# Kernel optimization log

Hardware: AMD Instinct MI355X
Metric: run time of the kernel (lower is better)

Reference implementation:

```python
import jax, jax.numpy as jnp
import numpy as np

DIM = 64
LSH_NUM_PROJS = 7
BLOCK_SIZE = 256
SAMPLE_SIZE = 256
MIN_SEQ_LEN = 2048


def _unit_hamming(n):
    # Gray-code-like permutation used by AngularLSH so adjacent hash ids differ by 1 bit
    a = np.arange(2)
    for i in range(1, n):
        a = np.concatenate([a, a[::-1] + 2 ** i])
    return jnp.asarray(a, dtype=jnp.int32)

_PERM = _unit_hamming(LSH_NUM_PROJS)                                  # [2^P]
_ENC = (2 ** jnp.arange(LSH_NUM_PROJS)).reshape(1, 1, 1, LSH_NUM_PROJS)


def _lsh_hash(mat, proj_dir):
    # mat: [b,h,n,d], proj_dir: [1,1,d,P] -> hash ids [b,h,n]
    mask = jnp.matmul(mat, proj_dir) > 0
    bin_ids = (mask * _ENC).sum(-1)
    return _PERM[bin_ids]


def _exact_attention(q, k, v, scale, causal=False, bias=None):
    qk = jnp.einsum('bhnd,bhmd->bhnm', q, k) * scale
    if causal:
        n, m = q.shape[2], k.shape[2]
        qk = qk + jnp.triu(jnp.full((n, m), jnp.finfo(q.dtype).min, q.dtype), 1)[None, None]
    if bias is not None:
        qk = qk + bias
    lse = jax.scipy.special.logsumexp(qk, axis=-1, keepdims=True)      # [b,h,n,1]
    out = jnp.einsum('bhnm,bhmd->bhnd', jnp.exp(qk - lse), v)
    return out, lse


def _add_attn(a1, l1, a2, l2):
    c = (1.0 / (1.0 + jnp.exp(l2 - l1))).astype(a1.dtype)
    attn = c * a1 + (1 - c) * a2
    lse = l1 - jnp.log(c + jnp.finfo(l1.dtype).eps)
    return attn, lse


def _indexing(x, idx, chunk_size=-1):
    # x: [b,h,n,d], idx: [b,h,s] -> [b,h,s,d] (padded up to a multiple of chunk_size)
    g = jnp.take_along_axis(x, idx[..., None], axis=2)
    n = g.shape[2]
    if chunk_size > 0 and n % chunk_size != 0:
        pad = -n % chunk_size
        g = jnp.pad(g, ((0, 0), (0, 0), (0, pad), (0, 0)))
    return g


def _no_causal(q, k, v, scale, proj_dir, level):
    b, h, n_q, d = q.shape
    n_k = k.shape[2]
    if MIN_SEQ_LEN > n_q:
        return _exact_attention(q, k, v, scale, causal=False)
    q_idx = jnp.argsort(_lsh_hash(q, proj_dir), axis=2)
    k_idx = jnp.argsort(_lsh_hash(k, proj_dir), axis=2)
    q_idx_inv = jnp.argsort(q_idx, axis=2)
    kbs = BLOCK_SIZE
    q_s = _indexing(q, q_idx, kbs)
    k_s = _indexing(k, k_idx, kbs)
    v_s = _indexing(v, k_idx, kbs)
    num_blocks = k_s.shape[2] // kbs
    qbs = q_s.shape[2] // num_blocks
    # block-diagonal attention over LSH-sorted buckets
    q_blk = q_s.reshape(-1, 1, qbs, d)
    k_blk = k_s.reshape(-1, 1, kbs, d)
    v_blk = v_s.reshape(-1, 1, kbs, d)
    attn_block, lse_block = _exact_attention(q_blk, k_blk, v_blk, scale, causal=False)
    attn_block = attn_block.reshape(b, h, q_s.shape[2], -1)
    lse_block = lse_block.reshape(b, h, q_s.shape[2], -1)
    if q_s.shape[2] != n_q:
        attn_block = attn_block[:, :, :n_q, :]
        lse_block = lse_block[:, :, :n_q, :]
        q_s = q_s[:, :, :n_q, :]
        k_s = k_s[:, :, :n_k, :]
        v_s = v_s[:, :, :n_k, :]
    S = SAMPLE_SIZE
    if S > 0 and n_q > qbs and n_k > kbs:
        rng = jax.random.fold_in(jax.random.key(42), level)
        sampled = jax.random.randint(rng, (b, h, S), 0, n_k)
        v_sub = _indexing(v_s, sampled)
        k_sub = _indexing(k_s, sampled)
        offset = jnp.arange(n_q)[None, :, None]                         # (1,n,1)
        bm = (offset // qbs) == (sampled // kbs).reshape(-1, 1, S)      # (b*h,n,S)
        bias = bm.reshape(b, h, n_q, S).astype(q_s.dtype) * jnp.finfo(q_s.dtype).min
        attn_res, lse_res = _exact_attention(q_s, k_sub, v_sub, scale, causal=False, bias=bias)
        lse_res = lse_res + jnp.asarray(np.log(n_k / S), lse_res.dtype)
        attn, lse = _add_attn(attn_block, lse_block, attn_res, lse_res)
    else:
        attn, lse = attn_block, lse_block
    attn = _indexing(attn, q_idx_inv)
    lse = _indexing(lse, q_idx_inv)
    return attn, lse


def _hyper(q, k, v, scale, proj_dir, level=0):
    b, h, n_k, d = k.shape
    n_q = q.shape[2]
    if n_k <= MIN_SEQ_LEN:
        return _exact_attention(q, k, v, scale, causal=True)
    # recursive causal split: block-diagonal halves + un-masked lower-left quadrant
    q_bd = q.reshape(b, 2 * h, n_q // 2, d)
    k_bd = k.reshape(b, 2 * h, n_k // 2, d)
    v_bd = v.reshape(b, 2 * h, n_k // 2, d)
    attn_bd, lse_bd = _hyper(q_bd, k_bd, v_bd, scale, proj_dir, level + 1)
    attn_bd = attn_bd.reshape(b, h, -1, d)
    lse_bd = lse_bd.reshape(b, h, -1, 1)
    a_un, l_un = _no_causal(q[:, :, n_k // 2:, :], k[:, :, :n_k // 2, :],
                            v[:, :, :n_k // 2, :], scale, proj_dir, 100 + level)
    a_up, l_up = attn_bd[:, :, :n_q // 2, :], lse_bd[:, :, :n_q // 2, :]
    a_dn, l_dn = _add_attn(attn_bd[:, :, n_q // 2:, :], lse_bd[:, :, n_q // 2:, :], a_un, l_un)
    return jnp.concatenate([a_up, a_dn], axis=2), jnp.concatenate([l_up, l_dn], axis=2)


def setup_inputs() -> dict:
    rng = jax.random.key(0)
    kq, kk, kv, kp = jax.random.split(rng, 4)
    B, H, N, D = 1, 8, 8192, 64
    return {
        'query': jax.random.normal(kq, (B, H, N, D), jnp.float32),
        'key': jax.random.normal(kk, (B, H, N, D), jnp.float32),
        'value': jax.random.normal(kv, (B, H, N, D), jnp.float32),
        'proj_dir': jax.random.normal(kp, (1, 1, D, LSH_NUM_PROJS), jnp.float32),
    }


def reference(query, key, value, proj_dir):
    scale = query.shape[-1] ** -0.5
    attn, lse = _hyper(query, key, value, scale, proj_dir)
    return attn
```

## Files before the change

kernel.cpp:

```cpp
#include <hip/hip_runtime.h>
#include <stdint.h>
#include <math.h>

#define H 8
#define NSEQ 8192
#define D 64
#define SC2 0.18033688011112042f
#define LN2F 0.69314718055994531f
#define THR2 10.0f
#define EPSF 1.1920928955078125e-07f

typedef short v8s __attribute__((ext_vector_type(8)));
typedef float v4f __attribute__((ext_vector_type(4)));
typedef unsigned short ushort_t;

#define MFMA16(a,b,c) __builtin_amdgcn_mfma_f32_16x16x32_bf16((a),(b),(c),0,0,0)
#define SWZ(row, cb)    (((row)*128) + ((cb) ^ ((((row)&7))<<4)))
#define SWZ256(row, cb) (((row)*256) + ((cb) ^ ((((row)&7))<<4)))

__device__ __forceinline__ float exp2x(float x){
  float r; asm("v_exp_f32 %0, %1" : "=v"(r) : "v"(x)); return r;
}
__device__ __forceinline__ unsigned int cvtpk(float a, float b){
  unsigned int r; asm("v_cvt_pk_bf16_f32 %0, %1, %2" : "=v"(r) : "v"(a), "v"(b)); return r;
}
__device__ __forceinline__ ushort_t f2bf(float f){
  union { float f; unsigned int u; } c; c.f = f;
  unsigned int u = c.u + 0x7FFFu + ((c.u >> 16) & 1u);
  return (ushort_t)(u >> 16);
}
#define VONES (v8s){0x3F80,0x3F80,0x3F80,0x3F80,0x3F80,0x3F80,0x3F80,0x3F80}

__global__ __launch_bounds__(256) void prep_hash(
    const float* __restrict__ q, const float* __restrict__ k, const float* __restrict__ v,
    const float* __restrict__ proj,
    ushort_t* __restrict__ qb, ushort_t* __restrict__ kb, ushort_t* __restrict__ vb,
    int* __restrict__ hq, int* __restrict__ hk)
{
  __shared__ float tile[64][65];
  __shared__ float pj[448];
  __shared__ int pbuf[4][64];
  const int bid = blockIdx.x;
  const int t = threadIdx.x;
  if (bid >= 2048){
    const int tix = bid - 2048;
    size_t off = (size_t)tix*4096 + t*16;
    float4 f0 = *(const float4*)(v + off);
    float4 f1 = *(const float4*)(v + off + 4);
    float4 f2 = *(const float4*)(v + off + 8);
    float4 f3 = *(const float4*)(v + off + 12);
    uint4 o0, o1;
    o0.x = cvtpk(f0.x, f0.y);  o0.y = cvtpk(f0.z, f0.w);
    o0.z = cvtpk(f1.x, f1.y);  o0.w = cvtpk(f1.z, f1.w);
    o1.x = cvtpk(f2.x, f2.y);  o1.y = cvtpk(f2.z, f2.w);
    o1.z = cvtpk(f3.x, f3.y);  o1.w = cvtpk(f3.z, f3.w);
    *(uint4*)(vb + off) = o0;
    *(uint4*)(vb + off + 8) = o1;
    return;
  }
  const int isk = bid & 1;
  const int tix = bid >> 1;
  const int rowbase = tix << 6;
  const float* src = isk ? k : q;
  ushort_t* dstb = isk ? kb : qb;
  int* dsth = isk ? hk : hq;
  for (int i = t; i < 448; i += 256) pj[i] = proj[i];
  {
    const int r = t >> 2, cg = (t & 3) << 4;
    const float* s = src + (size_t)(rowbase + r)*64 + cg;
    float4 f0 = *(const float4*)(s);
    float4 f1 = *(const float4*)(s + 4);
    float4 f2 = *(const float4*)(s + 8);
    float4 f3 = *(const float4*)(s + 12);
    tile[r][cg+0]=f0.x;  tile[r][cg+1]=f0.y;  tile[r][cg+2]=f0.z;  tile[r][cg+3]=f0.w;
    tile[r][cg+4]=f1.x;  tile[r][cg+5]=f1.y;  tile[r][cg+6]=f1.z;  tile[r][cg+7]=f1.w;
    tile[r][cg+8]=f2.x;  tile[r][cg+9]=f2.y;  tile[r][cg+10]=f2.z; tile[r][cg+11]=f2.w;
    tile[r][cg+12]=f3.x; tile[r][cg+13]=f3.y; tile[r][cg+14]=f3.z; tile[r][cg+15]=f3.w;
    uint4 o0, o1;
    o0.x = cvtpk(f0.x, f0.y);  o0.y = cvtpk(f0.z, f0.w);
    o0.z = cvtpk(f1.x, f1.y);  o0.w = cvtpk(f1.z, f1.w);
    o1.x = cvtpk(f2.x, f2.y);  o1.y = cvtpk(f2.z, f2.w);
    o1.z = cvtpk(f3.x, f3.y);  o1.w = cvtpk(f3.z, f3.w);
    *(uint4*)(dstb + (size_t)(rowbase + r)*64 + cg) = o0;
    *(uint4*)(dstb + (size_t)(rowbase + r)*64 + cg + 8) = o1;
  }
  __syncthreads();
  {
    const int r = t & 63, pg = t >> 6;
    const int p2 = (pg < 3) ? (pg + 4) : 6;
    float d0 = 0.0f, d1 = 0.0f;
    for (int d = 0; d < 64; ++d){
      float x = tile[r][d];
      d0 = fmaf(x, pj[d*7 + pg], d0);
      d1 = fmaf(x, pj[d*7 + p2], d1);
    }
    int pb = (d0 > 0.0f ? (1 << pg) : 0);
    if (pg < 3 && d1 > 0.0f) pb |= (1 << (pg + 4));
    pbuf[pg][r] = pb;
  }
  __syncthreads();
  if (t < 64){
    int b = pbuf[0][t] | pbuf[1][t] | pbuf[2][t] | pbuf[3][t];
    dsth[rowbase + t] = b ^ (b >> 1);
  }
}

__device__ __forceinline__ void tf2x32(uint32_t k0, uint32_t k1,
                                       uint32_t x0, uint32_t x1,
                                       uint32_t& o0, uint32_t& o1)
{
  uint32_t ks0 = k0, ks1 = k1, ks2 = k0 ^ k1 ^ 0x1BD11BDAu;
  x0 += ks0; x1 += ks1;
#define RND(r) { x0 += x1; x1 = (x1 << (r)) | (x1 >> (32-(r))); x1 ^= x0; }
  RND(13) RND(15) RND(26) RND(6)  x0 += ks1; x1 += ks2 + 1u;
  RND(17) RND(29) RND(16) RND(24) x0 += ks2; x1 += ks0 + 2u;
  RND(13) RND(15) RND(26) RND(6)  x0 += ks0; x1 += ks1 + 3u;
  RND(17) RND(29) RND(16) RND(24) x0 += ks1; x1 += ks2 + 4u;
  RND(13) RND(15) RND(26) RND(6)  x0 += ks2; x1 += ks0 + 5u;
#undef RND
  o0 = x0; o1 = x1;
}

__device__ __forceinline__ void qk8(const v8s qf[2], const char* Ks, int lo, int hi, v4f sa[8]){
  __builtin_amdgcn_s_setprio(1);
#pragma unroll
  for (int st = 0; st < 8; ++st){
#pragma unroll
    for (int kc = 0; kc < 2; ++kc){
      v8s bf = *(const v8s*)(Ks + SWZ(st*16 + lo, kc*64 + hi*16));
      sa[st] = MFMA16(qf[kc], bf, sa[st]);
    }
  }
  __builtin_amdgcn_s_setprio(0);
}

__device__ __forceinline__ void sm_pv8s(v4f sa[8], char* Pw, const char* VTs,
                                        int lo, int hi, float m[4], v4f o[5]){
  float tm[4];
  bool grow = false;
#pragma unroll
  for (int reg = 0; reg < 4; ++reg){
    float a = fmaxf(fmaxf(sa[0][reg], sa[1][reg]), fmaxf(sa[2][reg], sa[3][reg]));
    float b = fmaxf(fmaxf(sa[4][reg], sa[5][reg]), fmaxf(sa[6][reg], sa[7][reg]));
    tm[reg] = fmaxf(a, b);
    grow = grow || (tm[reg] > m[reg] + THR2);
  }
  if (__any(grow)){
#pragma unroll
    for (int reg = 0; reg < 4; ++reg){
      float t = tm[reg];
      t = fmaxf(t, __shfl_xor(t, 1));
      t = fmaxf(t, __shfl_xor(t, 2));
      t = fmaxf(t, __shfl_xor(t, 4));
      t = fmaxf(t, __shfl_xor(t, 8));
      float mn = fmaxf(m[reg], t);
      float corr = exp2x(m[reg] - mn);
      m[reg] = mn;
#pragma unroll
      for (int dt = 0; dt < 5; ++dt) o[dt][reg] *= corr;
    }
  }
#pragma unroll
  for (int hh = 0; hh < 2; ++hh){
#pragma unroll
    for (int reg = 0; reg < 4; ++reg){
      float mr = m[reg];
      uint2 pw;
      pw.x = cvtpk(exp2x(sa[hh*4+0][reg]-mr), exp2x(sa[hh*4+1][reg]-mr));
      pw.y = cvtpk(exp2x(sa[hh*4+2][reg]-mr), exp2x(sa[hh*4+3][reg]-mr));
      *(uint2*)(Pw + SWZ(hi*4 + reg, 8*lo)) = pw;
    }
    asm volatile("" ::: "memory");
    __builtin_amdgcn_s_setprio(1);
#pragma unroll
    for (int kb = 0; kb < 2; ++kb){
      v8s pa = *(const v8s*)(Pw + SWZ(lo, kb*64 + hi*16));
#pragma unroll
      for (int dt = 0; dt < 4; ++dt){
        v8s vbr = *(const v8s*)(VTs + SWZ256(dt*16 + lo, hh*128 + kb*64 + hi*16));
        o[dt] = MFMA16(pa, vbr, o[dt]);
      }
      o[4] = MFMA16(pa, VONES, o[4]);
    }
    __builtin_amdgcn_s_setprio(0);
    asm volatile("" ::: "memory");
  }
}

__device__ __forceinline__ void vt_write_h(char* VTs, uint2 vr0, uint2 vr1, uint2 vr2, uint2 vr3,
                                           int vdg, int vlo, int vsth){
  const int cb = vsth*128 + vlo*8;
  uint2 w;
  w.x = (vr0.x & 0xFFFFu) | ((vr1.x & 0xFFFFu) << 16);
  w.y = (vr2.x & 0xFFFFu) | ((vr3.x & 0xFFFFu) << 16);
  *(uint2*)(VTs + SWZ256(vdg*4 + 0, cb)) = w;
  w.x = (vr0.x >> 16) | (vr1.x & 0xFFFF0000u);
  w.y = (vr2.x >> 16) | (vr3.x & 0xFFFF0000u);
  *(uint2*)(VTs + SWZ256(vdg*4 + 1, cb)) = w;
  w.x = (vr0.y & 0xFFFFu) | ((vr1.y & 0xFFFFu) << 16);
  w.y = (vr2.y & 0xFFFFu) | ((vr3.y & 0xFFFFu) << 16);
  *(uint2*)(VTs + SWZ256(vdg*4 + 2, cb)) = w;
  w.x = (vr0.y >> 16) | (vr1.y & 0xFFFF0000u);
  w.y = (vr2.y >> 16) | (vr3.y & 0xFFFF0000u);
  *(uint2*)(VTs + SWZ256(vdg*4 + 3, cb)) = w;
}

__global__ __launch_bounds__(512, 4) void diag_sort(
    const ushort_t* __restrict__ qb, const ushort_t* __restrict__ kb, const ushort_t* __restrict__ vb,
    float* __restrict__ out, float* __restrict__ lse,
    const int* __restrict__ hq, const int* __restrict__ hk,
    int* __restrict__ q100, int* __restrict__ k100,
    int* __restrict__ q101, int* __restrict__ k101,
    int* __restrict__ s100, int* __restrict__ s101)
{
  __shared__ __align__(16) char lds[49664];
  const int bid0 = blockIdx.x;
  const int tid = threadIdx.x;

  if (bid0 < 48){
    unsigned char  (*hist)[128] = (unsigned char (*)[128])lds;
    unsigned short (*off )[128] = (unsigned short(*)[128])(lds + 16384);
    int* bstart = (int*)(lds + 49152);
    const int t = tid;
    if (t < 128){
      int gid = bid0*128 + t;
      int level, span, idx; int* outp;
      if (gid < 2048){ level = 100; span = 4096; outp = s100; idx = gid; }
      else           { level = 101; span = 2048; outp = s101; idx = gid - 2048; }
      uint32_t r0, r1; tf2x32(0u, 42u, 0u, (uint32_t)level, r0, r1);
      uint32_t k20, k21; tf2x32(r0, r1, 0u, 1u, k20, k21);
      uint32_t o0, o1; tf2x32(k20, k21, 0u, (uint32_t)idx, o0, o1);
      outp[idx] = (int)((o0 ^ o1) % (uint32_t)span);
    }
    const int* src = nullptr; int n = 0, base = 0; int* outp = nullptr;
    if (bid0 < 8)       { int h = bid0;     src = hq + h*NSEQ + 4096;        n = 4096; base = 4096;          outp = q100 + h*4096; }
    else if (bid0 < 16) { int h = bid0 - 8; src = hk + h*NSEQ;               n = 4096; base = 0;             outp = k100 + h*4096; }
    else if (bid0 < 32) { int id = bid0-16; int h = id>>1, p = id&1;
                          src = hq + h*NSEQ + p*4096 + 2048;                 n = 2048; base = p*4096 + 2048; outp = q101 + id*2048; }
    else                { int id = bid0-32; int h = id>>1, p = id&1;
                          src = hk + h*NSEQ + p*4096;                        n = 2048; base = p*4096;       outp = k101 + id*2048; }
    const int chunk = n >> 7;
    if (t < 128) for (int b = 0; b < 128; ++b) hist[t][b] = 0;
    __syncthreads();
    const int* mysrc = src + (t & 127) * chunk;
    if (t < 128) for (int i = 0; i < chunk; ++i) hist[t][mysrc[i]]++;
    __syncthreads();
    if (t < 128){
      int s = 0;
      for (int tt = 0; tt < 128; ++tt) s += hist[tt][t];
      bstart[t] = s;
    }
    __syncthreads();
    if (t == 0){
      int run = 0;
      for (int b = 0; b < 128; ++b){ int c = bstart[b]; bstart[b] = run; run += c; }
    }
    __syncthreads();
    if (t < 128){
      unsigned int run = (unsigned int)bstart[t];
      for (int tt = 0; tt < 128; ++tt){ off[tt][t] = (unsigned short)run; run += hist[tt][t]; }
    }
    __syncthreads();
    if (t < 128){
      for (int i = 0; i < chunk; ++i){
        int hsh = mysrc[i];
        unsigned short pos = off[t][hsh]++;
        outp[pos] = base + t * chunk + i;
      }
    }
    return;
  }

  char* Ks  = lds;
  char* VTs = lds + 16384;
  char* Ps  = lds + 32768;
  const int bid = bid0 - 48;
  const int xcd = bid & 7, sl = bid >> 3;
  const int inst = xcd*4 + (sl >> 4);
  const int pi = sl & 15;
  const int h = inst >> 2, tblk = inst & 3;
  const size_t hoff = (size_t)h * NSEQ * D;
  const ushort_t* qh = qb + hoff; const ushort_t* kh = kb + hoff; const ushort_t* vh = vb + hoff;
  const int blkbase = tblk * 2048;
  const int w = tid >> 6, lane = tid & 63;
  const int lo = lane & 15, hi = lane >> 4;
  char* Pw = Ps + w*2048;
  const int kr = tid >> 2, kq = tid & 3;
  const int vlo = tid & 15, vdg = (tid >> 4) & 15, vsth = tid >> 8;

  const int qt  = (w < 4) ? (31 - pi) : pi;
  const int wq  = w & 3;
  const int nkt   = (31 - pi)/2 + 1;
  const int mynkt = qt/2 + 1;
  const int qpos0 = qt*64 + wq*16;

  v8s qf[2];
  {
    const ushort_t* r = qh + (size_t)(blkbase + qpos0 + lo) * D;
    qf[0] = *(const v8s*)(r + hi*8);
    qf[1] = *(const v8s*)(r + 32 + hi*8);
  }
  const v4f vz = {0.0f, 0.0f, 0.0f, 0.0f};
  v4f o[5] = {vz, vz, vz, vz, vz};
  float m[4] = {-INFINITY, -INFINITY, -INFINITY, -INFINITY};

  uint4 kreg0, kreg1; uint2 vr0, vr1, vr2, vr3;
#define DLOAD(kt) { \
    const ushort_t* ksr = kh + (size_t)(blkbase + (kt)*128 + kr)*D + kq*16; \
    kreg0 = *(const uint4*)ksr; \
    kreg1 = *(const uint4*)(ksr + 8); \
    const ushort_t* vs = vh + (size_t)(blkbase + (kt)*128 + vsth*64 + vlo)*D + vdg*4; \
    vr0 = *(const uint2*)(vs); \
    vr1 = *(const uint2*)(vs + 16*D); \
    vr2 = *(const uint2*)(vs + 32*D); \
    vr3 = *(const uint2*)(vs + 48*D); }

  DLOAD(0);
#pragma unroll 1
  for (int kt = 0; kt < nkt; ++kt){
    *(uint4*)(Ks + SWZ(kr, kq*32))      = kreg0;
    *(uint4*)(Ks + SWZ(kr, kq*32 + 16)) = kreg1;
    vt_write_h(VTs, vr0, vr1, vr2, vr3, vdg, vlo, vsth);
    __syncthreads();
    if (kt + 1 < nkt) DLOAD(kt+1);
    if (kt < mynkt){
      v4f sa[8] = {vz, vz, vz, vz, vz, vz, vz, vz};
      qk8(qf, Ks, lo, hi, sa);
#pragma unroll
      for (int st = 0; st < 8; ++st) sa[st] *= SC2;
      if (kt == mynkt - 1){
#pragma unroll
        for (int st = 0; st < 8; ++st){
          int kpos = kt*128 + st*16 + lo;
#pragma unroll
          for (int reg = 0; reg < 4; ++reg)
            if (kpos > qpos0 + hi*4 + reg) sa[st][reg] = -INFINITY;
        }
      }
      sm_pv8s(sa, Pw, VTs, lo, hi, m, o);
    }
    __syncthreads();
  }
#undef DLOAD
#pragma unroll
  for (int reg = 0; reg < 4; ++reg){
    int rw = blkbase + qpos0 + hi*4 + reg;
    float lsum = o[4][reg];
    float inv = 1.0f / lsum;
#pragma unroll
    for (int dt = 0; dt < 4; ++dt)
      out[hoff + (size_t)rw*D + dt*16 + lo] = o[dt][reg] * inv;
    if (lo == 0) lse[h*NSEQ + rw] = m[reg]*LN2F + logf(lsum);
  }
}

__device__ __forceinline__ int nc_key(const int* __restrict__ ki, const int* __restrict__ sp,
                                      int qblk, int kt, int pos, int& msk){
  if (kt < 2){ msk = 0; return ki[qblk*256 + kt*128 + pos]; }
  int s = sp[(kt-2)*128 + pos]; msk = ((s >> 8) == qblk) ? 1 : 0; return ki[s];
}

__global__ __launch_bounds__(512, 4) void nc_both(
    const ushort_t* __restrict__ qb, const ushort_t* __restrict__ kb, const ushort_t* __restrict__ vb,
    float* __restrict__ out, float* __restrict__ lse,
    const int* __restrict__ q101, const int* __restrict__ k101, const int* __restrict__ s101,
    const int* __restrict__ q100, const int* __restrict__ k100, const int* __restrict__ s100,
    ushort_t* __restrict__ a100, float* __restrict__ lse100)
{
  __shared__ __align__(16) char Ks[16384];
  __shared__ __align__(16) char VTs[16384];
  __shared__ __align__(16) char Ps[8][2048];
  __shared__ int kmk[128];
  const int bid = blockIdx.x;
  const bool lvl101 = bid < 256;
  int inst, jb; float delta2; int seglen;
  const int *qi, *ki, *sp;
  if (lvl101){
    int xcd = bid & 7, sl = bid >> 3; inst = xcd*2 + (sl >> 4); jb = sl & 15;
    delta2 = 3.0f; seglen = 2048;
    qi = q101 + inst*seglen; ki = k101 + inst*seglen; sp = s101 + inst*256;
  } else {
    int b2 = bid - 256; inst = b2 & 7; jb = b2 >> 3;
    delta2 = 4.0f; seglen = 4096;
    qi = q100 + inst*seglen; ki = k100 + inst*seglen; sp = s100 + inst*256;
  }
  const int h = lvl101 ? (inst >> 1) : inst;
  const int qblk = jb >> 1;
  const size_t hoff = (size_t)h * NSEQ * D;
  const ushort_t* qh = qb + hoff; const ushort_t* kh = kb + hoff; const ushort_t* vh = vb + hoff;
  const int tid = threadIdx.x;
  const int w = tid >> 6, lane = tid & 63;
  const int lo = lane & 15, hi = lane >> 4;
  char* Pw = Ps[w];
  const int kr = tid >> 2, kq = tid & 3;
  const int vlo = tid & 15, vdg = (tid >> 4) & 15, vsth = tid >> 8;

  int orig[4];
  v8s qf[2];
  {
    int qrl = qi[jb*128 + w*16 + lo];
    const ushort_t* r = qh + (size_t)qrl * D;
    qf[0] = *(const v8s*)(r + hi*8);
    qf[1] = *(const v8s*)(r + 32 + hi*8);
#pragma unroll
    for (int reg = 0; reg < 4; ++reg) orig[reg] = qi[jb*128 + w*16 + hi*4 + reg];
  }
  const v4f vz = {0.0f, 0.0f, 0.0f, 0.0f};
  v4f o[5] = {vz, vz, vz, vz, vz};
  float m[4] = {-INFINITY, -INFINITY, -INFINITY, -INFINITY};

  uint4 kreg0, kreg1; uint2 vr0, vr1, vr2, vr3; int msk;
#define NLOAD(kt) { \
    int krow = nc_key(ki, sp, qblk, kt, kr, msk); \
    const ushort_t* ksr = kh + (size_t)krow*D + kq*16; \
    kreg0 = *(const uint4*)ksr; \
    kreg1 = *(const uint4*)(ksr + 8); \
    int m_; \
    int g0 = nc_key(ki, sp, qblk, kt, vsth*64 + vlo,      m_); \
    int g1 = nc_key(ki, sp, qblk, kt, vsth*64 + 16 + vlo, m_); \
    int g2 = nc_key(ki, sp, qblk, kt, vsth*64 + 32 + vlo, m_); \
    int g3 = nc_key(ki, sp, qblk, kt, vsth*64 + 48 + vlo, m_); \
    vr0 = *(const uint2*)(vh + (size_t)g0*D + vdg*4); \
    vr1 = *(const uint2*)(vh + (size_t)g1*D + vdg*4); \
    vr2 = *(const uint2*)(vh + (size_t)g2*D + vdg*4); \
    vr3 = *(const uint2*)(vh + (size_t)g3*D + vdg*4); }

  NLOAD(0);
#pragma unroll 1
  for (int kt = 0; kt < 4; ++kt){
    *(uint4*)(Ks + SWZ(kr, kq*32))      = kreg0;
    *(uint4*)(Ks + SWZ(kr, kq*32 + 16)) = kreg1;
    if (kq == 0) kmk[kr] = msk;
    vt_write_h(VTs, vr0, vr1, vr2, vr3, vdg, vlo, vsth);
    __syncthreads();
    if (kt + 1 < 4) NLOAD(kt+1);
    v4f sa[8] = {vz, vz, vz, vz, vz, vz, vz, vz};
    qk8(qf, Ks, lo, hi, sa);
    if (kt < 2){
#pragma unroll
      for (int st = 0; st < 8; ++st) sa[st] *= SC2;
    } else {
#pragma unroll
      for (int st = 0; st < 8; ++st){
        if (kmk[st*16 + lo]) sa[st] = (v4f){-INFINITY, -INFINITY, -INFINITY, -INFINITY};
        else                 sa[st] = sa[st]*SC2 + delta2;
      }
    }
    sm_pv8s(sa, Pw, VTs, lo, hi, m, o);
    __syncthreads();
  }
#undef NLOAD
  if (lvl101){
#pragma unroll
    for (int reg = 0; reg < 4; ++reg){
      int og = orig[reg];
      float lsum = o[4][reg];
      float l1v = lse[h*NSEQ + og];
      float l2v = m[reg]*LN2F + logf(lsum);
      float c = 1.0f / (1.0f + __expf(l2v - l1v));
      float inv = (1.0f - c) / lsum;
#pragma unroll
      for (int dt = 0; dt < 4; ++dt){
        float* ap = out + hoff + (size_t)og*D + dt*16 + lo;
        *ap = c * (*ap) + inv * o[dt][reg];
      }
      if (lo == 0) lse[h*NSEQ + og] = l1v - logf(c + EPSF);
    }
  } else {
#pragma unroll
    for (int reg = 0; reg < 4; ++reg){
      int og = orig[reg];
      float lsum = o[4][reg];
      float inv = 1.0f / lsum;
      ushort_t* arow = a100 + ((size_t)h*NSEQ + og)*D;
#pragma unroll
      for (int dt = 0; dt < 4; ++dt)
        arow[dt*16 + lo] = f2bf(o[dt][reg] * inv);
      if (lo == 0) lse100[h*NSEQ + og] = m[reg]*LN2F + logf(lsum);
    }
  }
}

__global__ __launch_bounds__(256) void merge_kernel(
    float* __restrict__ out, const float* __restrict__ lse,
    const ushort_t* __restrict__ a100, const float* __restrict__ lse100)
{
  const int gid = blockIdx.x * 256 + threadIdx.x;
  const size_t e = (size_t)gid * 4;
  const int h = (int)(e >> 18);
  const int rem = (int)(e & 262143);
  const int og = 4096 + (rem >> 6);
  const size_t row = (size_t)h*NSEQ + og;
  const float l1 = lse[row];
  const float l2 = lse100[row];
  const float c = 1.0f / (1.0f + __expf(l2 - l1));
  const float ic = 1.0f - c;
  float* op = out + ((size_t)h*NSEQ*D) + (size_t)og*D + (rem & 63);
  float4 ov = *(float4*)op;
  uint2 av = *(const uint2*)(a100 + row*D + (rem & 63));
  float a0 = __uint_as_float((av.x & 0xFFFFu) << 16);
  float a1 = __uint_as_float((av.x & 0xFFFF0000u));
  float a2 = __uint_as_float((av.y & 0xFFFFu) << 16);
  float a3 = __uint_as_float((av.y & 0xFFFF0000u));
  ov.x = c*ov.x + ic*a0;
  ov.y = c*ov.y + ic*a1;
  ov.z = c*ov.z + ic*a2;
  ov.w = c*ov.w + ic*a3;
  *(float4*)op = ov;
}

extern "C" void kernel_launch(void* const* d_in, const int* in_sizes, int n_in,
                              void* d_out, int out_size, void* d_ws, size_t ws_size,
                              hipStream_t stream)
{
  const float* q    = (const float*)d_in[0];
  const float* k    = (const float*)d_in[1];
  const float* v    = (const float*)d_in[2];
  const float* proj = (const float*)d_in[3];
  float* out = (float*)d_out;

  char* ws = (char*)d_ws;
  float* lse = (float*)ws;
  int* hq   = (int*)(ws + 262144);
  int* hk   = (int*)(ws + 524288);
  int* q100 = (int*)(ws + 786432);
  int* k100 = (int*)(ws + 917504);
  int* q101 = (int*)(ws + 1048576);
  int* k101 = (int*)(ws + 1179648);
  int* s100 = (int*)(ws + 1310720);
  int* s101 = (int*)(ws + 1318912);
  ushort_t* qb = (ushort_t*)(ws + 1335296);
  ushort_t* kb = qb + (size_t)H*NSEQ*D;
  ushort_t* vb = kb + (size_t)H*NSEQ*D;
  ushort_t* a100 = vb + (size_t)H*NSEQ*D;
  float* lse100 = (float*)(a100 + (size_t)H*NSEQ*D);

  prep_hash    <<<dim3(3072), dim3(256), 0, stream>>>(q, k, v, proj, qb, kb, vb, hq, hk);
  diag_sort    <<<dim3(560),  dim3(512), 0, stream>>>(qb, kb, vb, out, lse, hq, hk,
                                                      q100, k100, q101, k101, s100, s101);
  nc_both      <<<dim3(512),  dim3(512), 0, stream>>>(qb, kb, vb, out, lse,
                                                      q101, k101, s101, q100, k100, s100,
                                                      a100, lse100);
  merge_kernel <<<dim3(2048), dim3(256), 0, stream>>>(out, lse, a100, lse100);
}
```

Baseline: 107.4 us.

## Prefetch key indices and masks into LDS, raise occupancy bound to 6

The nc_both kernel now loads all 512 key row indices (including the dependent sp->ki double gather for sampled keys) once into shared memory at kernel start, packing the same-block mask into the top bit. Each tile's K/V gather then reads indices from LDS instead of issuing dependent global loads, and the kmk mask array is dropped. Both kernels also raise launch_bounds min-blocks from 4 to 6, which may force fewer registers and risks spills. One extra __syncthreads is added before the main loop.

```diff
diff --git a/kernel.cpp b/kernel.cpp
--- a/kernel.cpp
+++ b/kernel.cpp
@@ -205,7 +205,7 @@
   *(uint2*)(VTs + SWZ256(vdg*4 + 3, cb)) = w;
 }
 
-__global__ __launch_bounds__(512, 4) void diag_sort(
+__global__ __launch_bounds__(512, 6) void diag_sort(
     const ushort_t* __restrict__ qb, const ushort_t* __restrict__ kb, const ushort_t* __restrict__ vb,
     float* __restrict__ out, float* __restrict__ lse,
     const int* __restrict__ hq, const int* __restrict__ hk,
@@ -354,13 +354,7 @@
   }
 }
 
-__device__ __forceinline__ int nc_key(const int* __restrict__ ki, const int* __restrict__ sp,
-                                      int qblk, int kt, int pos, int& msk){
-  if (kt < 2){ msk = 0; return ki[qblk*256 + kt*128 + pos]; }
-  int s = sp[(kt-2)*128 + pos]; msk = ((s >> 8) == qblk) ? 1 : 0; return ki[s];
-}
-
-__global__ __launch_bounds__(512, 4) void nc_both(
+__global__ __launch_bounds__(512, 6) void nc_both(
     const ushort_t* __restrict__ qb, const ushort_t* __restrict__ kb, const ushort_t* __restrict__ vb,
     float* __restrict__ out, float* __restrict__ lse,
     const int* __restrict__ q101, const int* __restrict__ k101, const int* __restrict__ s101,
@@ -370,7 +364,7 @@
   __shared__ __align__(16) char Ks[16384];
   __shared__ __align__(16) char VTs[16384];
   __shared__ __align__(16) char Ps[8][2048];
-  __shared__ int kmk[128];
+  __shared__ unsigned int ilds[512];
   const int bid = blockIdx.x;
   const bool lvl101 = bid < 256;
   int inst, jb; float delta2; int seglen;
@@ -395,6 +389,16 @@
   const int kr = tid >> 2, kq = tid & 3;
   const int vlo = tid & 15, vdg = (tid >> 4) & 15, vsth = tid >> 8;
 
+  {
+    if (tid < 256){
+      ilds[tid] = (unsigned int)ki[qblk*256 + tid];
+    } else {
+      int s = sp[tid - 256];
+      unsigned int krow = (unsigned int)ki[s];
+      if ((s >> 8) == qblk) krow |= 0x80000000u;
+      ilds[tid] = krow;
+    }
+  }
   int orig[4];
   v8s qf[2];
   {
@@ -408,18 +412,18 @@
   const v4f vz = {0.0f, 0.0f, 0.0f, 0.0f};
   v4f o[5] = {vz, vz, vz, vz, vz};
   float m[4] = {-INFINITY, -INFINITY, -INFINITY, -INFINITY};
-
-  uint4 kreg0, kreg1; uint2 vr0, vr1, vr2, vr3; int msk;
+  __syncthreads();
+
+  uint4 kreg0, kreg1; uint2 vr0, vr1, vr2, vr3;
 #define NLOAD(kt) { \
-    int krow = nc_key(ki, sp, qblk, kt, kr, msk); \
+    unsigned int krow = ilds[(kt)*128 + kr] & 0x7FFFFFFFu; \
     const ushort_t* ksr = kh + (size_t)krow*D + kq*16; \
     kreg0 = *(const uint4*)ksr; \
     kreg1 = *(const uint4*)(ksr + 8); \
-    int m_; \
-    int g0 = nc_key(ki, sp, qblk, kt, vsth*64 + vlo,      m_); \
-    int g1 = nc_key(ki, sp, qblk, kt, vsth*64 + 16 + vlo, m_); \
-    int g2 = nc_key(ki, sp, qblk, kt, vsth*64 + 32 + vlo, m_); \
-    int g3 = nc_key(ki, sp, qblk, kt, vsth*64 + 48 + vlo, m_); \
+    unsigned int g0 = ilds[(kt)*128 + vsth*64 + vlo     ] & 0x7FFFFFFFu; \
+    unsigned int g1 = ilds[(kt)*128 + vsth*64 + 16 + vlo] & 0x7FFFFFFFu; \
+    unsigned int g2 = ilds[(kt)*128 + vsth*64 + 32 + vlo] & 0x7FFFFFFFu; \
+    unsigned int g3 = ilds[(kt)*128 + vsth*64 + 48 + vlo] & 0x7FFFFFFFu; \
     vr0 = *(const uint2*)(vh + (size_t)g0*D + vdg*4); \
     vr1 = *(const uint2*)(vh + (size_t)g1*D + vdg*4); \
     vr2 = *(const uint2*)(vh + (size_t)g2*D + vdg*4); \
@@ -430,7 +434,6 @@
   for (int kt = 0; kt < 4; ++kt){
     *(uint4*)(Ks + SWZ(kr, kq*32))      = kreg0;
     *(uint4*)(Ks + SWZ(kr, kq*32 + 16)) = kreg1;
-    if (kq == 0) kmk[kr] = msk;
     vt_write_h(VTs, vr0, vr1, vr2, vr3, vdg, vlo, vsth);
     __syncthreads();
     if (kt + 1 < 4) NLOAD(kt+1);
@@ -442,8 +445,8 @@
     } else {
 #pragma unroll
       for (int st = 0; st < 8; ++st){
-        if (kmk[st*16 + lo]) sa[st] = (v4f){-INFINITY, -INFINITY, -INFINITY, -INFINITY};
-        else                 sa[st] = sa[st]*SC2 + delta2;
+        if (ilds[kt*128 + st*16 + lo] >> 31) sa[st] = (v4f){-INFINITY, -INFINITY, -INFINITY, -INFINITY};
+        else                                 sa[st] = sa[st]*SC2 + delta2;
       }
     }
     sm_pv8s(sa, Pw, VTs, lo, hi, m, o);
```

Result: slower. 219.0 us (+103.8%).
